# Performance work log

Measured on AMD Instinct MI355X. Metric: run time of the kernel, lower is better.

Reference implementation:

```python
import jax, jax.numpy as jnp
import numpy as np

X_DIM, Z_DIM, H_DIM, N_LAYERS = 128, 64, 512, 2
T, B = 128, 256
BETA = 1.0


def setup_inputs() -> dict:
    key = jax.random.key(0)
    ks = iter(jax.random.split(key, 64))
    def p(shape):
        return 0.05 * jax.random.normal(next(ks), shape, jnp.float32)
    d = {
        "x": jax.random.normal(next(ks), (T, B, X_DIM), jnp.float32),
        "eps": jax.random.normal(next(ks), (T, B, Z_DIM), jnp.float32),
        # phi_x: Linear(x,h) ReLU Linear(h,h) ReLU
        "phi_x_w1": p((H_DIM, X_DIM)), "phi_x_b1": p((H_DIM,)),
        "phi_x_w2": p((H_DIM, H_DIM)), "phi_x_b2": p((H_DIM,)),
        # phi_z: Linear(z,h) ReLU
        "phi_z_w": p((H_DIM, Z_DIM)), "phi_z_b": p((H_DIM,)),
        # enc: Linear(2h,h) ReLU Linear(h,h) ReLU; heads to z
        "enc_w1": p((H_DIM, 2 * H_DIM)), "enc_b1": p((H_DIM,)),
        "enc_w2": p((H_DIM, H_DIM)), "enc_b2": p((H_DIM,)),
        "enc_mu_w": p((Z_DIM, H_DIM)), "enc_mu_b": p((Z_DIM,)),
        "enc_lv_w": p((Z_DIM, H_DIM)), "enc_lv_b": p((Z_DIM,)),
        # prior: Linear(h,h) ReLU; heads to z
        "prior_w": p((H_DIM, H_DIM)), "prior_b": p((H_DIM,)),
        "prior_mu_w": p((Z_DIM, H_DIM)), "prior_mu_b": p((Z_DIM,)),
        "prior_lv_w": p((Z_DIM, H_DIM)), "prior_lv_b": p((Z_DIM,)),
        # dec: Linear(2h,h) ReLU Linear(h,h) ReLU; heads to x
        "dec_w1": p((H_DIM, 2 * H_DIM)), "dec_b1": p((H_DIM,)),
        "dec_w2": p((H_DIM, H_DIM)), "dec_b2": p((H_DIM,)),
        "dec_mu_w": p((X_DIM, H_DIM)), "dec_mu_b": p((X_DIM,)),
        "dec_lv_w": p((X_DIM, H_DIM)), "dec_lv_b": p((X_DIM,)),
        # GRU (bias=False): layer0 input 2h, layer1 input h
        "gru_wih0": p((3 * H_DIM, 2 * H_DIM)), "gru_whh0": p((3 * H_DIM, H_DIM)),
        "gru_wih1": p((3 * H_DIM, H_DIM)), "gru_whh1": p((3 * H_DIM, H_DIM)),
    }
    return d


def _lin(a, W, b):
    return a @ W.T + b


def _gru_cell(inp, h, Wih, Whh):
    gi = inp @ Wih.T  # [B, 3h]
    gh = h @ Whh.T
    i_r, i_z, i_n = jnp.split(gi, 3, axis=1)
    h_r, h_z, h_n = jnp.split(gh, 3, axis=1)
    r = jax.nn.sigmoid(i_r + h_r)
    zg = jax.nn.sigmoid(i_z + h_z)
    n = jnp.tanh(i_n + r * h_n)
    return (1.0 - zg) * n + zg * h


def reference(x, eps,
              phi_x_w1, phi_x_b1, phi_x_w2, phi_x_b2,
              phi_z_w, phi_z_b,
              enc_w1, enc_b1, enc_w2, enc_b2,
              enc_mu_w, enc_mu_b, enc_lv_w, enc_lv_b,
              prior_w, prior_b, prior_mu_w, prior_mu_b, prior_lv_w, prior_lv_b,
              dec_w1, dec_b1, dec_w2, dec_b2,
              dec_mu_w, dec_mu_b, dec_lv_w, dec_lv_b,
              gru_wih0, gru_whh0, gru_wih1, gru_whh1):
    Tn = x.shape[0]
    relu = jax.nn.relu

    def step(carry, xe):
        h, kld, rec = carry  # h: [N_LAYERS, B, H]
        x_t, eps_t = xe
        phi_x_t = relu(_lin(relu(_lin(x_t, phi_x_w1, phi_x_b1)), phi_x_w2, phi_x_b2))
        h_last = h[-1]
        enc_h = relu(_lin(relu(_lin(jnp.concatenate([phi_x_t, h_last], axis=1), enc_w1, enc_b1)), enc_w2, enc_b2))
        mu_q = _lin(enc_h, enc_mu_w, enc_mu_b)
        logvar_q = jnp.clip(_lin(enc_h, enc_lv_w, enc_lv_b), -6.0, 6.0)
        pri_h = relu(_lin(h_last, prior_w, prior_b))
        mu_p = _lin(pri_h, prior_mu_w, prior_mu_b)
        logvar_p = jnp.clip(_lin(pri_h, prior_lv_w, prior_lv_b), -6.0, 6.0)
        z_t = mu_q + eps_t * jnp.exp(0.5 * logvar_q)
        phi_z_t = relu(_lin(z_t, phi_z_w, phi_z_b))
        dec_h = relu(_lin(relu(_lin(jnp.concatenate([phi_z_t, h_last], axis=1), dec_w1, dec_b1)), dec_w2, dec_b2))
        dec_mu = _lin(dec_h, dec_mu_w, dec_mu_b)
        dec_lv = jnp.clip(_lin(dec_h, dec_lv_w, dec_lv_b), -6.0, 6.0)
        rnn_in = jnp.concatenate([phi_x_t, phi_z_t], axis=1)
        h0 = _gru_cell(rnn_in, h[0], gru_wih0, gru_whh0)
        h1 = _gru_cell(h0, h[1], gru_wih1, gru_whh1)
        h_new = jnp.stack([h0, h1])
        kl = 0.5 * jnp.sum(logvar_p - logvar_q + (jnp.exp(logvar_q) + (mu_q - mu_p) ** 2) / jnp.exp(logvar_p) - 1.0, axis=1)
        nll = 0.5 * jnp.sum(dec_lv + (x_t - dec_mu) ** 2 / jnp.exp(dec_lv), axis=1)
        return (h_new, kld + kl.mean(), rec + nll.mean()), None

    h0 = jnp.zeros((N_LAYERS, x.shape[1], H_DIM), x.dtype)
    (h_f, kld, rec), _ = jax.lax.scan(step, (h0, jnp.zeros((), x.dtype), jnp.zeros((), x.dtype)), (x, eps))
    total = (BETA * kld + rec) / Tn
    return total, rec / Tn, kld / Tn
```

## Files before the change

### kernel.cpp

```cpp
#include <hip/hip_runtime.h>
#include <hip/hip_bf16.h>

typedef __attribute__((ext_vector_type(4))) float f32x4;
typedef __attribute__((ext_vector_type(8))) short bf16x8;
typedef unsigned short u16;

#define DEV static __device__ __forceinline__

DEV u16 f2bf(float f){
  unsigned v = __float_as_uint(f);
  v += 0x7fffu + ((v >> 16) & 1u);
  return (u16)(v >> 16);
}
DEV float bf2f(u16 u){ return __uint_as_float(((unsigned)u) << 16); }
DEV float sigm(float x){ return 1.0f / (1.0f + __expf(-x)); }
DEV float tanh_(float x){ return 1.0f - 2.0f / (__expf(2.0f * x) + 1.0f); }
DEV bf16x8 ld8(const u16* p){ return *(const bf16x8*)p; }

struct GemmDesc {
  const u16* A; const u16* A2; const u16* W;
  const float* bias; void* out;
  int lda, lda2, ldw, ldo, N, K, K2, flags;
};
struct GemmMulti { GemmDesc d[4]; int nblk[4]; int ndesc; };

template<int NT>
DEV void mm_acc(const u16* ap, const u16* wp, int ldw, int K, f32x4* acc){
  for (int k = 0; k < K; k += 32){
    bf16x8 a = ld8(ap + k);
    #pragma unroll
    for (int nt = 0; nt < NT; ++nt){
      bf16x8 b = ld8(wp + (size_t)(nt * 16) * ldw + k);
      acc[nt] = __builtin_amdgcn_mfma_f32_16x16x32_bf16(a, b, acc[nt], 0, 0, 0);
    }
  }
}

DEV void run_gemm(const GemmDesc& d, int blk){
  const int ntn = d.N >> 6;
  const int bm = blk / ntn, bn = blk - bm * ntn;
  const int w = threadIdx.x >> 6, lane = threadIdx.x & 63;
  const int r = lane & 15, g = lane >> 4;
  const int m0 = bm * 64 + w * 16, n0 = bn * 64;
  f32x4 acc[4];
  #pragma unroll
  for (int i = 0; i < 4; ++i) acc[i] = (f32x4){0.f, 0.f, 0.f, 0.f};
  mm_acc<4>(d.A + (size_t)(m0 + r) * d.lda + g * 8,
            d.W + (size_t)(n0 + r) * d.ldw + g * 8, d.ldw, d.K, acc);
  if (d.A2)
    mm_acc<4>(d.A2 + (size_t)(m0 + r) * d.lda2 + g * 8,
              d.W + (size_t)(n0 + r) * d.ldw + d.K + g * 8, d.ldw, d.K2, acc);
  #pragma unroll
  for (int nt = 0; nt < 4; ++nt){
    #pragma unroll
    for (int i = 0; i < 4; ++i){
      const int row = m0 + g * 4 + i, col = n0 + nt * 16 + r;
      float v = acc[nt][i];
      if (d.bias) v += d.bias[col];
      if (d.flags & 1) v = fmaxf(v, 0.f);
      if (d.flags & 2) ((u16*)d.out)[(size_t)row * d.ldo + col] = f2bf(v);
      else             ((float*)d.out)[(size_t)row * d.ldo + col] = v;
    }
  }
}

__global__ __launch_bounds__(256) void k_gemm_multi(GemmMulti gm){
  int blk = blockIdx.x, di = 0;
  while (di < gm.ndesc - 1 && blk >= gm.nblk[di]){ blk -= gm.nblk[di]; ++di; }
  run_gemm(gm.d[di], blk);
}

#define NCONV 19
struct ConvMulti { const float* src[NCONV]; u16* dst[NCONV]; int n[NCONV]; int total; };

__global__ __launch_bounds__(256) void k_convert(ConvMulti cm){
  const int stride = gridDim.x * blockDim.x;
  for (int i = blockIdx.x * blockDim.x + threadIdx.x; i < cm.total; i += stride){
    int idx = i, di = 0;
    while (idx >= cm.n[di]){ idx -= cm.n[di]; ++di; }
    cm.dst[di][idx] = f2bf(cm.src[di][idx]);
  }
}

__global__ __launch_bounds__(256) void k_enc_fused(
    const u16* __restrict__ enc_h1, const u16* __restrict__ pri_h,
    const u16* __restrict__ enc_w2, const float* __restrict__ enc_b2,
    const u16* __restrict__ enc_mu_w, const float* __restrict__ enc_mu_b,
    const u16* __restrict__ enc_lv_w, const float* __restrict__ enc_lv_b,
    const u16* __restrict__ pri_mu_w, const float* __restrict__ pri_mu_b,
    const u16* __restrict__ pri_lv_w, const float* __restrict__ pri_lv_b,
    const u16* __restrict__ phi_z_w, const float* __restrict__ phi_z_b,
    const float* __restrict__ eps_t, u16* __restrict__ phi_z_out,
    float* __restrict__ kld_acc)
{
  __shared__ u16 enc_h_s[16 * 528];
  __shared__ float head_s[4][16 * 64];
  __shared__ u16 z_s[16 * 72];
  __shared__ float red[256];
  const int tid = threadIdx.x;
  const int w = tid >> 6, lane = tid & 63, r = lane & 15, g = lane >> 4;
  const int m0 = blockIdx.x * 16;

  {
    f32x4 acc[8];
    #pragma unroll
    for (int i = 0; i < 8; ++i) acc[i] = (f32x4){0.f, 0.f, 0.f, 0.f};
    const int n0 = w * 128;
    mm_acc<8>(enc_h1 + (size_t)(m0 + r) * 512 + g * 8,
              enc_w2 + (size_t)(n0 + r) * 512 + g * 8, 512, 512, acc);
    #pragma unroll
    for (int nt = 0; nt < 8; ++nt)
      #pragma unroll
      for (int i = 0; i < 4; ++i){
        const int row = g * 4 + i, col = n0 + nt * 16 + r;
        float v = fmaxf(acc[nt][i] + enc_b2[col], 0.f);
        enc_h_s[row * 528 + col] = f2bf(v);
      }
  }
  __syncthreads();
  {
    f32x4 acc[4];
    #pragma unroll
    for (int i = 0; i < 4; ++i) acc[i] = (f32x4){0.f, 0.f, 0.f, 0.f};
    const u16* ap; int lda; const u16* W; const float* bias; bool clip;
    if      (w == 0){ ap = enc_h_s;                      lda = 528; W = enc_mu_w; bias = enc_mu_b; clip = false; }
    else if (w == 1){ ap = enc_h_s;                      lda = 528; W = enc_lv_w; bias = enc_lv_b; clip = true;  }
    else if (w == 2){ ap = pri_h + (size_t)m0 * 512;     lda = 512; W = pri_mu_w; bias = pri_mu_b; clip = false; }
    else            { ap = pri_h + (size_t)m0 * 512;     lda = 512; W = pri_lv_w; bias = pri_lv_b; clip = true;  }
    mm_acc<4>(ap + (size_t)r * lda + g * 8, W + (size_t)r * 512 + g * 8, 512, 512, acc);
    #pragma unroll
    for (int nt = 0; nt < 4; ++nt)
      #pragma unroll
      for (int i = 0; i < 4; ++i){
        const int row = g * 4 + i, col = nt * 16 + r;
        float v = acc[nt][i] + bias[col];
        if (clip) v = fminf(fmaxf(v, -6.f), 6.f);
        head_s[w][row * 64 + col] = v;
      }
  }
  __syncthreads();
  float klsum = 0.f;
  for (int e = tid; e < 1024; e += 256){
    const int row = e >> 6, col = e & 63;
    const float qm = head_s[0][e], qv = head_s[1][e];
    const float pm = head_s[2][e], pv = head_s[3][e];
    const float zv = qm + eps_t[(size_t)(m0 + row) * 64 + col] * __expf(0.5f * qv);
    z_s[row * 72 + col] = f2bf(zv);
    const float dm = qm - pm;
    klsum += 0.5f * (pv - qv + (__expf(qv) + dm * dm) * __expf(-pv) - 1.0f);
  }
  red[tid] = klsum;
  __syncthreads();
  for (int s = 128; s > 0; s >>= 1){ if (tid < s) red[tid] += red[tid + s]; __syncthreads(); }
  if (tid == 0) atomicAdd(kld_acc, red[0]);
  {
    f32x4 acc[8];
    #pragma unroll
    for (int i = 0; i < 8; ++i) acc[i] = (f32x4){0.f, 0.f, 0.f, 0.f};
    const int n0 = w * 128;
    mm_acc<8>(z_s + (size_t)r * 72 + g * 8,
              phi_z_w + (size_t)(n0 + r) * 64 + g * 8, 64, 64, acc);
    #pragma unroll
    for (int nt = 0; nt < 8; ++nt)
      #pragma unroll
      for (int i = 0; i < 4; ++i){
        const int row = m0 + g * 4 + i, col = n0 + nt * 16 + r;
        float v = fmaxf(acc[nt][i] + phi_z_b[col], 0.f);
        phi_z_out[(size_t)row * 512 + col] = f2bf(v);
      }
  }
}

__global__ __launch_bounds__(256) void k_l5(GemmMulti gm,
    const float* __restrict__ gi0, const float* __restrict__ gh0, u16* __restrict__ h0)
{
  if ((int)blockIdx.x < gm.nblk[0]){ run_gemm(gm.d[0], blockIdx.x); return; }
  const int b = blockIdx.x - gm.nblk[0];
  for (int idx = b * 256 + threadIdx.x; idx < 256 * 512; idx += 16 * 256){
    const int row = idx >> 9, col = idx & 511;
    const float* gi = gi0 + (size_t)row * 1536;
    const float* gh = gh0 + (size_t)row * 1536;
    const float rr = sigm(gi[col] + gh[col]);
    const float zg = sigm(gi[col + 512] + gh[col + 512]);
    const float nn = tanh_(gi[col + 1024] + rr * gh[col + 1024]);
    const float hv = (1.f - zg) * nn + zg * bf2f(h0[idx]);
    h0[idx] = f2bf(hv);
  }
}

__global__ __launch_bounds__(256) void k_l6(GemmMulti gm,
    const u16* __restrict__ dec_h,
    const u16* __restrict__ dmu_w, const float* __restrict__ dmu_b,
    const u16* __restrict__ dlv_w, const float* __restrict__ dlv_b,
    const float* __restrict__ x_t, float* __restrict__ rec_acc)
{
  __shared__ float dmu_s[16 * 128], dlv_s[16 * 128];
  __shared__ float red[256];
  if ((int)blockIdx.x < gm.nblk[0]){ run_gemm(gm.d[0], blockIdx.x); return; }
  const int wg = blockIdx.x - gm.nblk[0];
  const int m0 = wg * 16;
  const int tid = threadIdx.x, w = tid >> 6, lane = tid & 63, r = lane & 15, g = lane >> 4;
  {
    f32x4 acc[4];
    #pragma unroll
    for (int i = 0; i < 4; ++i) acc[i] = (f32x4){0.f, 0.f, 0.f, 0.f};
    const u16* W = (w & 2) ? dlv_w : dmu_w;
    const float* bias = (w & 2) ? dlv_b : dmu_b;
    const int n0 = (w & 1) * 64;
    const bool clip = (w & 2);
    mm_acc<4>(dec_h + (size_t)(m0 + r) * 512 + g * 8,
              W + (size_t)(n0 + r) * 512 + g * 8, 512, 512, acc);
    #pragma unroll
    for (int nt = 0; nt < 4; ++nt)
      #pragma unroll
      for (int i = 0; i < 4; ++i){
        const int row = g * 4 + i, col = n0 + nt * 16 + r;
        float v = acc[nt][i] + bias[col];
        if (clip) v = fminf(fmaxf(v, -6.f), 6.f);
        (clip ? dlv_s : dmu_s)[row * 128 + col] = v;
      }
  }
  __syncthreads();
  float ns = 0.f;
  for (int e = tid; e < 2048; e += 256){
    const int row = e >> 7, col = e & 127;
    const float mu = dmu_s[e], lv = dlv_s[e];
    const float xv = x_t[(size_t)(m0 + row) * 128 + col];
    const float d = xv - mu;
    ns += 0.5f * (lv + d * d * __expf(-lv));
  }
  red[tid] = ns;
  __syncthreads();
  for (int s = 128; s > 0; s >>= 1){ if (tid < s) red[tid] += red[tid + s]; __syncthreads(); }
  if (tid == 0) atomicAdd(rec_acc, red[0]);
}

__global__ __launch_bounds__(256) void k_l7(const float* __restrict__ gi1,
    const float* __restrict__ gh1, u16* __restrict__ h1,
    int dofinal, const float* __restrict__ accf, float* __restrict__ out)
{
  if ((int)blockIdx.x < 16){
    for (int idx = blockIdx.x * 256 + threadIdx.x; idx < 256 * 512; idx += 16 * 256){
      const int row = idx >> 9, col = idx & 511;
      const float* gi = gi1 + (size_t)row * 1536;
      const float* gh = gh1 + (size_t)row * 1536;
      const float rr = sigm(gi[col] + gh[col]);
      const float zg = sigm(gi[col + 512] + gh[col + 512]);
      const float nn = tanh_(gi[col + 1024] + rr * gh[col + 1024]);
      const float hv = (1.f - zg) * nn + zg * bf2f(h1[idx]);
      h1[idx] = f2bf(hv);
    }
  } else if (dofinal && threadIdx.x == 0){
    const float kl = accf[0] * (1.f / 32768.f);
    const float rc = accf[1] * (1.f / 32768.f);
    out[0] = rc + kl; out[1] = rc; out[2] = kl;
  }
}

extern "C" void kernel_launch(void* const* d_in, const int* in_sizes, int n_in,
                              void* d_out, int out_size, void* d_ws, size_t ws_size,
                              hipStream_t stream)
{
  (void)in_sizes; (void)n_in; (void)out_size; (void)ws_size;
  const float* x     = (const float*)d_in[0];
  const float* eps   = (const float*)d_in[1];
  const float* w_px1 = (const float*)d_in[2];
  const float* b_px1 = (const float*)d_in[3];
  const float* w_px2 = (const float*)d_in[4];
  const float* b_px2 = (const float*)d_in[5];
  const float* w_pz  = (const float*)d_in[6];
  const float* b_pz  = (const float*)d_in[7];
  const float* w_e1  = (const float*)d_in[8];
  const float* b_e1  = (const float*)d_in[9];
  const float* w_e2  = (const float*)d_in[10];
  const float* b_e2  = (const float*)d_in[11];
  const float* w_emu = (const float*)d_in[12];
  const float* b_emu = (const float*)d_in[13];
  const float* w_elv = (const float*)d_in[14];
  const float* b_elv = (const float*)d_in[15];
  const float* w_pr  = (const float*)d_in[16];
  const float* b_pr  = (const float*)d_in[17];
  const float* w_pmu = (const float*)d_in[18];
  const float* b_pmu = (const float*)d_in[19];
  const float* w_plv = (const float*)d_in[20];
  const float* b_plv = (const float*)d_in[21];
  const float* w_d1  = (const float*)d_in[22];
  const float* b_d1  = (const float*)d_in[23];
  const float* w_d2  = (const float*)d_in[24];
  const float* b_d2  = (const float*)d_in[25];
  const float* w_dmu = (const float*)d_in[26];
  const float* b_dmu = (const float*)d_in[27];
  const float* w_dlv = (const float*)d_in[28];
  const float* b_dlv = (const float*)d_in[29];
  const float* w_ih0 = (const float*)d_in[30];
  const float* w_hh0 = (const float*)d_in[31];
  const float* w_ih1 = (const float*)d_in[32];
  const float* w_hh1 = (const float*)d_in[33];

  char* base = (char*)d_ws;
  size_t off = 0;
  auto alloc = [&](size_t bytes)->char*{
    char* p = base + off;
    off = (off + bytes + 255) & ~(size_t)255;
    return p;
  };
  u16* xbf    = (u16*)alloc((size_t)4194304 * 2);
  u16* cb_px1 = (u16*)alloc((size_t)65536 * 2);
  u16* cb_px2 = (u16*)alloc((size_t)262144 * 2);
  u16* cb_pz  = (u16*)alloc((size_t)32768 * 2);
  u16* cb_e1  = (u16*)alloc((size_t)524288 * 2);
  u16* cb_e2  = (u16*)alloc((size_t)262144 * 2);
  u16* cb_emu = (u16*)alloc((size_t)32768 * 2);
  u16* cb_elv = (u16*)alloc((size_t)32768 * 2);
  u16* cb_pr  = (u16*)alloc((size_t)262144 * 2);
  u16* cb_pmu = (u16*)alloc((size_t)32768 * 2);
  u16* cb_plv = (u16*)alloc((size_t)32768 * 2);
  u16* cb_d1  = (u16*)alloc((size_t)524288 * 2);
  u16* cb_d2  = (u16*)alloc((size_t)262144 * 2);
  u16* cb_dmu = (u16*)alloc((size_t)65536 * 2);
  u16* cb_dlv = (u16*)alloc((size_t)65536 * 2);
  u16* cb_ih0 = (u16*)alloc((size_t)1572864 * 2);
  u16* cb_hh0 = (u16*)alloc((size_t)786432 * 2);
  u16* cb_ih1 = (u16*)alloc((size_t)786432 * 2);
  u16* cb_hh1 = (u16*)alloc((size_t)786432 * 2);
  u16* phiX   = (u16*)alloc((size_t)16777216 * 2);
  const size_t mark = off;
  u16* phiX1  = (u16*)alloc((size_t)16777216 * 2);
  off = mark;
  u16* a_ench1 = (u16*)alloc((size_t)131072 * 2);
  u16* a_prih  = (u16*)alloc((size_t)131072 * 2);
  u16* a_phiz  = (u16*)alloc((size_t)131072 * 2);
  u16* a_dech1 = (u16*)alloc((size_t)131072 * 2);
  u16* a_dech  = (u16*)alloc((size_t)131072 * 2);
  float* gh0 = (float*)alloc((size_t)393216 * 4);
  float* gh1 = (float*)alloc((size_t)393216 * 4);
  float* gi0 = (float*)alloc((size_t)393216 * 4);
  float* gi1 = (float*)alloc((size_t)393216 * 4);
  u16* h0 = (u16*)alloc((size_t)131072 * 2);
  u16* h1 = (u16*)alloc((size_t)131072 * 2);
  float* accf = (float*)alloc(256);

  hipMemsetAsync(h0, 0, (size_t)131072 * 2 * 2 + 256, stream);

  ConvMulti cm; int ci = 0, tot = 0;
  auto addc = [&](const float* s, u16* d, int n){ cm.src[ci] = s; cm.dst[ci] = d; cm.n[ci] = n; ++ci; tot += n; };
  addc(x, xbf, 4194304);
  addc(w_px1, cb_px1, 65536);   addc(w_px2, cb_px2, 262144);
  addc(w_pz,  cb_pz,  32768);   addc(w_e1,  cb_e1,  524288);
  addc(w_e2,  cb_e2,  262144);  addc(w_emu, cb_emu, 32768);
  addc(w_elv, cb_elv, 32768);   addc(w_pr,  cb_pr,  262144);
  addc(w_pmu, cb_pmu, 32768);   addc(w_plv, cb_plv, 32768);
  addc(w_d1,  cb_d1,  524288);  addc(w_d2,  cb_d2,  262144);
  addc(w_dmu, cb_dmu, 65536);   addc(w_dlv, cb_dlv, 65536);
  addc(w_ih0, cb_ih0, 1572864); addc(w_hh0, cb_hh0, 786432);
  addc(w_ih1, cb_ih1, 786432);  addc(w_hh1, cb_hh1, 786432);
  cm.total = tot;
  k_convert<<<2048, 256, 0, stream>>>(cm);

  auto D = [](const u16* A, int lda, const u16* A2, int lda2, const u16* W, int ldw,
              const float* bias, void* out, int ldo, int N, int K, int K2, int flags)->GemmDesc{
    GemmDesc d; d.A = A; d.A2 = A2; d.W = W; d.bias = bias; d.out = out;
    d.lda = lda; d.lda2 = lda2; d.ldw = ldw; d.ldo = ldo;
    d.N = N; d.K = K; d.K2 = K2; d.flags = flags; return d;
  };

  {
    GemmMulti g; g.ndesc = 1;
    g.d[0] = D(xbf, 128, nullptr, 0, cb_px1, 128, b_px1, phiX1, 512, 512, 128, 0, 3);
    g.nblk[0] = 512 * 8;
    k_gemm_multi<<<512 * 8, 256, 0, stream>>>(g);
    g.d[0] = D(phiX1, 512, nullptr, 0, cb_px2, 512, b_px2, phiX, 512, 512, 512, 0, 3);
    k_gemm_multi<<<512 * 8, 256, 0, stream>>>(g);
  }

  for (int t = 0; t < 128; ++t){
    const u16* phiXt  = phiX + (size_t)t * 131072;
    const float* epst = eps  + (size_t)t * 16384;
    const float* xt   = x    + (size_t)t * 32768;

    GemmMulti g1; g1.ndesc = 4;
    g1.d[0] = D(phiXt, 512, h1, 512, cb_e1, 1024, b_e1, a_ench1, 512, 512, 512, 512, 3); g1.nblk[0] = 32;
    g1.d[1] = D(h1, 512, nullptr, 0, cb_pr, 512, b_pr, a_prih, 512, 512, 512, 0, 3);     g1.nblk[1] = 32;
    g1.d[2] = D(h1, 512, nullptr, 0, cb_hh1, 512, nullptr, gh1, 1536, 1536, 512, 0, 0);  g1.nblk[2] = 96;
    g1.d[3] = D(h0, 512, nullptr, 0, cb_hh0, 512, nullptr, gh0, 1536, 1536, 512, 0, 0);  g1.nblk[3] = 96;
    k_gemm_multi<<<256, 256, 0, stream>>>(g1);

    k_enc_fused<<<16, 256, 0, stream>>>(a_ench1, a_prih, cb_e2, b_e2,
        cb_emu, b_emu, cb_elv, b_elv, cb_pmu, b_pmu, cb_plv, b_plv,
        cb_pz, b_pz, epst, a_phiz, accf + 0);

    GemmMulti g4; g4.ndesc = 2;
    g4.d[0] = D(a_phiz, 512, h1, 512, cb_d1, 1024, b_d1, a_dech1, 512, 512, 512, 512, 3);  g4.nblk[0] = 32;
    g4.d[1] = D(phiXt, 512, a_phiz, 512, cb_ih0, 1024, nullptr, gi0, 1536, 1536, 512, 512, 0); g4.nblk[1] = 96;
    k_gemm_multi<<<128, 256, 0, stream>>>(g4);

    GemmMulti g5; g5.ndesc = 1;
    g5.d[0] = D(a_dech1, 512, nullptr, 0, cb_d2, 512, b_d2, a_dech, 512, 512, 512, 0, 3); g5.nblk[0] = 32;
    k_l5<<<48, 256, 0, stream>>>(g5, gi0, gh0, h0);

    GemmMulti g6; g6.ndesc = 1;
    g6.d[0] = D(h0, 512, nullptr, 0, cb_ih1, 512, nullptr, gi1, 1536, 1536, 512, 0, 0); g6.nblk[0] = 96;
    k_l6<<<112, 256, 0, stream>>>(g6, a_dech, cb_dmu, b_dmu, cb_dlv, b_dlv, xt, accf + 1);

    k_l7<<<17, 256, 0, stream>>>(gi1, gh1, h1, (t == 127) ? 1 : 0, accf, (float*)d_out);
  }
}
```

Before: 21.51 ms.

## Fuse the whole VRNN time loop into one persistent per-batch-tile kernel

Replaces the roughly seven kernel launches per timestep with a single persistent kernel. Each of 16 blocks owns 16 batch rows and loops over all 128 timesteps, keeping intermediate activations in shared memory and fusing both GRU gate GEMMs with their elementwise updates. Hidden states are double-buffered in global memory, so no grid-wide synchronisation is needed. This removes launch overhead and the global round-trips for gate pre-activations. The cost is that only 16 workgroups run, so every block streams all weights from cache at each step, which may leave most of the GPU idle and make the kernel cache-bandwidth bound.

```diff
diff --git a/kernel.cpp b/kernel.cpp
--- a/kernel.cpp
+++ b/kernel.cpp
@@ -16,58 +16,53 @@
 DEV float sigm(float x){ return 1.0f / (1.0f + __expf(-x)); }
 DEV float tanh_(float x){ return 1.0f - 2.0f / (__expf(2.0f * x) + 1.0f); }
 DEV bf16x8 ld8(const u16* p){ return *(const bf16x8*)p; }
-
-struct GemmDesc {
-  const u16* A; const u16* A2; const u16* W;
-  const float* bias; void* out;
-  int lda, lda2, ldw, ldo, N, K, K2, flags;
-};
-struct GemmMulti { GemmDesc d[4]; int nblk[4]; int ndesc; };
-
-template<int NT>
-DEV void mm_acc(const u16* ap, const u16* wp, int ldw, int K, f32x4* acc){
-  for (int k = 0; k < K; k += 32){
-    bf16x8 a = ld8(ap + k);
+DEV float clip6(float v){ return fminf(fmaxf(v, -6.f), 6.f); }
+
+template<int KIT, int NT>
+DEV void mmK(const u16* ap, const u16* wp, int ldw, f32x4* acc){
+  #pragma unroll 4
+  for (int kk = 0; kk < KIT; ++kk){
+    bf16x8 a = ld8(ap + kk * 32);
     #pragma unroll
     for (int nt = 0; nt < NT; ++nt){
-      bf16x8 b = ld8(wp + (size_t)(nt * 16) * ldw + k);
+      bf16x8 b = ld8(wp + (size_t)(nt * 16) * ldw + kk * 32);
       acc[nt] = __builtin_amdgcn_mfma_f32_16x16x32_bf16(a, b, acc[nt], 0, 0, 0);
     }
   }
 }
 
-DEV void run_gemm(const GemmDesc& d, int blk){
+struct GemmDesc {
+  const u16* A; const u16* W; const float* bias; u16* out;
+  int lda, ldw, ldo, N, K;
+};
+
+__global__ __launch_bounds__(256) void k_gemm_pre(GemmDesc d){
   const int ntn = d.N >> 6;
-  const int bm = blk / ntn, bn = blk - bm * ntn;
+  const int bm = blockIdx.x / ntn, bn = blockIdx.x - bm * ntn;
   const int w = threadIdx.x >> 6, lane = threadIdx.x & 63;
   const int r = lane & 15, g = lane >> 4;
   const int m0 = bm * 64 + w * 16, n0 = bn * 64;
   f32x4 acc[4];
   #pragma unroll
   for (int i = 0; i < 4; ++i) acc[i] = (f32x4){0.f, 0.f, 0.f, 0.f};
-  mm_acc<4>(d.A + (size_t)(m0 + r) * d.lda + g * 8,
-            d.W + (size_t)(n0 + r) * d.ldw + g * 8, d.ldw, d.K, acc);
-  if (d.A2)
-    mm_acc<4>(d.A2 + (size_t)(m0 + r) * d.lda2 + g * 8,
-              d.W + (size_t)(n0 + r) * d.ldw + d.K + g * 8, d.ldw, d.K2, acc);
+  const u16* ap = d.A + (size_t)(m0 + r) * d.lda + g * 8;
+  const u16* wp = d.W + (size_t)(n0 + r) * d.ldw + g * 8;
+  for (int k = 0; k < d.K; k += 32){
+    bf16x8 a = ld8(ap + k);
+    #pragma unroll
+    for (int nt = 0; nt < 4; ++nt){
+      bf16x8 b = ld8(wp + (size_t)(nt * 16) * d.ldw + k);
+      acc[nt] = __builtin_amdgcn_mfma_f32_16x16x32_bf16(a, b, acc[nt], 0, 0, 0);
+    }
+  }
   #pragma unroll
-  for (int nt = 0; nt < 4; ++nt){
+  for (int nt = 0; nt < 4; ++nt)
     #pragma unroll
     for (int i = 0; i < 4; ++i){
       const int row = m0 + g * 4 + i, col = n0 + nt * 16 + r;
-      float v = acc[nt][i];
-      if (d.bias) v += d.bias[col];
-      if (d.flags & 1) v = fmaxf(v, 0.f);
-      if (d.flags & 2) ((u16*)d.out)[(size_t)row * d.ldo + col] = f2bf(v);
-      else             ((float*)d.out)[(size_t)row * d.ldo + col] = v;
-    }
-  }
-}
-
-__global__ __launch_bounds__(256) void k_gemm_multi(GemmMulti gm){
-  int blk = blockIdx.x, di = 0;
-  while (di < gm.ndesc - 1 && blk >= gm.nblk[di]){ blk -= gm.nblk[di]; ++di; }
-  run_gemm(gm.d[di], blk);
+      float v = fmaxf(acc[nt][i] + d.bias[col], 0.f);
+      d.out[(size_t)row * d.ldo + col] = f2bf(v);
+    }
 }
 
 #define NCONV 19
@@ -82,177 +77,250 @@
   }
 }
 
-__global__ __launch_bounds__(256) void k_enc_fused(
-    const u16* __restrict__ enc_h1, const u16* __restrict__ pri_h,
-    const u16* __restrict__ enc_w2, const float* __restrict__ enc_b2,
-    const u16* __restrict__ enc_mu_w, const float* __restrict__ enc_mu_b,
-    const u16* __restrict__ enc_lv_w, const float* __restrict__ enc_lv_b,
-    const u16* __restrict__ pri_mu_w, const float* __restrict__ pri_mu_b,
-    const u16* __restrict__ pri_lv_w, const float* __restrict__ pri_lv_b,
-    const u16* __restrict__ phi_z_w, const float* __restrict__ phi_z_b,
-    const float* __restrict__ eps_t, u16* __restrict__ phi_z_out,
-    float* __restrict__ kld_acc)
+struct Params {
+  const u16 *phiX, *e1, *pr, *e2, *emu, *elv, *pmu, *plv, *pz, *d1, *ih0, *hh0, *ih1, *hh1, *d2, *dmu, *dlv;
+  const float *b_e1, *b_pr, *b_e2, *b_emu, *b_elv, *b_pmu, *b_plv, *b_pz, *b_d1, *b_d2, *b_dmu, *b_dlv;
+  const float *eps, *x;
+  u16 *h0a, *h0b, *h1a, *h1b;
+  float *accf;
+};
+
+#define HP 520
+
+__global__ __launch_bounds__(256, 1) void k_vrnn16(Params P)
 {
-  __shared__ u16 enc_h_s[16 * 528];
-  __shared__ float head_s[4][16 * 64];
-  __shared__ u16 z_s[16 * 72];
+  const int tid = threadIdx.x, w = tid >> 6, lane = tid & 63;
+  const int r = lane & 15, g = lane >> 4;
+  const int bid = blockIdx.x, m0 = bid * 16;
+  const int n0w = w * 128;
+
+  __shared__ u16 ench1_s[16 * HP], prih_s[16 * HP], phiz_s[16 * HP], dech1_s[16 * HP], dh_s[16 * HP];
+  __shared__ float fbuf[4096];
+  __shared__ u16 zs[16 * 72];
   __shared__ float red[256];
-  const int tid = threadIdx.x;
-  const int w = tid >> 6, lane = tid & 63, r = lane & 15, g = lane >> 4;
-  const int m0 = blockIdx.x * 16;
-
-  {
-    f32x4 acc[8];
-    #pragma unroll
-    for (int i = 0; i < 8; ++i) acc[i] = (f32x4){0.f, 0.f, 0.f, 0.f};
-    const int n0 = w * 128;
-    mm_acc<8>(enc_h1 + (size_t)(m0 + r) * 512 + g * 8,
-              enc_w2 + (size_t)(n0 + r) * 512 + g * 8, 512, 512, acc);
-    #pragma unroll
-    for (int nt = 0; nt < 8; ++nt)
-      #pragma unroll
-      for (int i = 0; i < 4; ++i){
-        const int row = g * 4 + i, col = n0 + nt * 16 + r;
-        float v = fmaxf(acc[nt][i] + enc_b2[col], 0.f);
-        enc_h_s[row * 528 + col] = f2bf(v);
+  float* qmu_s = fbuf;        float* qlv_s = fbuf + 1024;
+  float* pmu_s = fbuf + 2048; float* plv_s = fbuf + 3072;
+  float* dmu_s = fbuf;        float* dlv_s = fbuf + 2048;
+
+  float klacc = 0.f, nllacc = 0.f;
+
+  for (int t = 0; t < 128; ++t){
+    const u16* h1o = (t & 1) ? P.h1b : P.h1a;  u16* h1n = (t & 1) ? P.h1a : P.h1b;
+    const u16* h0o = (t & 1) ? P.h0b : P.h0a;  u16* h0n = (t & 1) ? P.h0a : P.h0b;
+    const u16* aX  = P.phiX + ((size_t)t * 256 + m0 + r) * 512 + g * 8;
+    const u16* aH1 = h1o + (size_t)(m0 + r) * 512 + g * 8;
+    const u16* aH0 = h0o + (size_t)(m0 + r) * 512 + g * 8;
+
+    { f32x4 acc[8];
+      #pragma unroll
+      for (int i = 0; i < 8; ++i) acc[i] = (f32x4){0.f,0.f,0.f,0.f};
+      mmK<16,8>(aX,  P.e1 + (size_t)(n0w + r) * 1024 + g * 8, 1024, acc);
+      mmK<16,8>(aH1, P.e1 + (size_t)(n0w + r) * 1024 + 512 + g * 8, 1024, acc);
+      #pragma unroll
+      for (int nt = 0; nt < 8; ++nt)
+        #pragma unroll
+        for (int i = 0; i < 4; ++i){
+          const int row = g * 4 + i, col = n0w + nt * 16 + r;
+          ench1_s[row * HP + col] = f2bf(fmaxf(acc[nt][i] + P.b_e1[col], 0.f));
+        }
+    }
+    { f32x4 acc[8];
+      #pragma unroll
+      for (int i = 0; i < 8; ++i) acc[i] = (f32x4){0.f,0.f,0.f,0.f};
+      mmK<16,8>(aH1, P.pr + (size_t)(n0w + r) * 512 + g * 8, 512, acc);
+      #pragma unroll
+      for (int nt = 0; nt < 8; ++nt)
+        #pragma unroll
+        for (int i = 0; i < 4; ++i){
+          const int row = g * 4 + i, col = n0w + nt * 16 + r;
+          prih_s[row * HP + col] = f2bf(fmaxf(acc[nt][i] + P.b_pr[col], 0.f));
+        }
+    }
+    __syncthreads();
+    { f32x4 acc[8];
+      #pragma unroll
+      for (int i = 0; i < 8; ++i) acc[i] = (f32x4){0.f,0.f,0.f,0.f};
+      mmK<16,8>(ench1_s + r * HP + g * 8, P.e2 + (size_t)(n0w + r) * 512 + g * 8, 512, acc);
+      #pragma unroll
+      for (int nt = 0; nt < 8; ++nt)
+        #pragma unroll
+        for (int i = 0; i < 4; ++i){
+          const int row = g * 4 + i, col = n0w + nt * 16 + r;
+          dh_s[row * HP + col] = f2bf(fmaxf(acc[nt][i] + P.b_e2[col], 0.f));
+        }
+    }
+    __syncthreads();
+    { f32x4 acc[4];
+      #pragma unroll
+      for (int i = 0; i < 4; ++i) acc[i] = (f32x4){0.f,0.f,0.f,0.f};
+      const u16* A  = (w < 2) ? dh_s : prih_s;
+      const u16* W_ = (w == 0) ? P.emu : (w == 1) ? P.elv : (w == 2) ? P.pmu : P.plv;
+      const float* bs = (w == 0) ? P.b_emu : (w == 1) ? P.b_elv : (w == 2) ? P.b_pmu : P.b_plv;
+      float* outp = (w == 0) ? qmu_s : (w == 1) ? qlv_s : (w == 2) ? pmu_s : plv_s;
+      const bool cl = (w & 1);
+      mmK<16,4>(A + r * HP + g * 8, W_ + (size_t)r * 512 + g * 8, 512, acc);
+      #pragma unroll
+      for (int nt = 0; nt < 4; ++nt)
+        #pragma unroll
+        for (int i = 0; i < 4; ++i){
+          const int row = g * 4 + i, col = nt * 16 + r;
+          float v = acc[nt][i] + bs[col];
+          if (cl) v = clip6(v);
+          outp[row * 64 + col] = v;
+        }
+    }
+    __syncthreads();
+    { const float* epst = P.eps + (size_t)t * 16384 + (size_t)m0 * 64;
+      for (int e = tid; e < 1024; e += 256){
+        const int row = e >> 6, col = e & 63;
+        const float qm = qmu_s[e], qv = qlv_s[e];
+        const float pm = pmu_s[e], pv = plv_s[e];
+        const float zv = qm + epst[row * 64 + col] * __expf(0.5f * qv);
+        zs[row * 72 + col] = f2bf(zv);
+        const float dm = qm - pm;
+        klacc += 0.5f * (pv - qv + (__expf(qv) + dm * dm) * __expf(-pv) - 1.f);
       }
-  }
-  __syncthreads();
-  {
-    f32x4 acc[4];
-    #pragma unroll
-    for (int i = 0; i < 4; ++i) acc[i] = (f32x4){0.f, 0.f, 0.f, 0.f};
-    const u16* ap; int lda; const u16* W; const float* bias; bool clip;
-    if      (w == 0){ ap = enc_h_s;                      lda = 528; W = enc_mu_w; bias = enc_mu_b; clip = false; }
-    else if (w == 1){ ap = enc_h_s;                      lda = 528; W = enc_lv_w; bias = enc_lv_b; clip = true;  }
-    else if (w == 2){ ap = pri_h + (size_t)m0 * 512;     lda = 512; W = pri_mu_w; bias = pri_mu_b; clip = false; }
-    else            { ap = pri_h + (size_t)m0 * 512;     lda = 512; W = pri_lv_w; bias = pri_lv_b; clip = true;  }
-    mm_acc<4>(ap + (size_t)r * lda + g * 8, W + (size_t)r * 512 + g * 8, 512, 512, acc);
-    #pragma unroll
-    for (int nt = 0; nt < 4; ++nt)
-      #pragma unroll
-      for (int i = 0; i < 4; ++i){
-        const int row = g * 4 + i, col = nt * 16 + r;
-        float v = acc[nt][i] + bias[col];
-        if (clip) v = fminf(fmaxf(v, -6.f), 6.f);
-        head_s[w][row * 64 + col] = v;
+    }
+    __syncthreads();
+    { f32x4 acc[8];
+      #pragma unroll
+      for (int i = 0; i < 8; ++i) acc[i] = (f32x4){0.f,0.f,0.f,0.f};
+      mmK<2,8>(zs + r * 72 + g * 8, P.pz + (size_t)(n0w + r) * 64 + g * 8, 64, acc);
+      #pragma unroll
+      for (int nt = 0; nt < 8; ++nt)
+        #pragma unroll
+        for (int i = 0; i < 4; ++i){
+          const int row = g * 4 + i, col = n0w + nt * 16 + r;
+          phiz_s[row * HP + col] = f2bf(fmaxf(acc[nt][i] + P.b_pz[col], 0.f));
+        }
+    }
+    __syncthreads();
+    { f32x4 acc[8];
+      #pragma unroll
+      for (int i = 0; i < 8; ++i) acc[i] = (f32x4){0.f,0.f,0.f,0.f};
+      mmK<16,8>(phiz_s + r * HP + g * 8, P.d1 + (size_t)(n0w + r) * 1024 + g * 8, 1024, acc);
+      mmK<16,8>(aH1, P.d1 + (size_t)(n0w + r) * 1024 + 512 + g * 8, 1024, acc);
+      #pragma unroll
+      for (int nt = 0; nt < 8; ++nt)
+        #pragma unroll
+        for (int i = 0; i < 4; ++i){
+          const int row = g * 4 + i, col = n0w + nt * 16 + r;
+          dech1_s[row * HP + col] = f2bf(fmaxf(acc[nt][i] + P.b_d1[col], 0.f));
+        }
+    }
+    { const u16* aZ = phiz_s + r * HP + g * 8;
+      for (int j = 0; j < 2; ++j){
+        f32x4 gi[3][4], gh[3][4];
+        #pragma unroll
+        for (int gt = 0; gt < 3; ++gt)
+          #pragma unroll
+          for (int i = 0; i < 4; ++i){ gi[gt][i] = (f32x4){0.f,0.f,0.f,0.f}; gh[gt][i] = (f32x4){0.f,0.f,0.f,0.f}; }
+        #pragma unroll
+        for (int gt = 0; gt < 3; ++gt){
+          const u16* wih = P.ih0 + (size_t)(gt * 512 + n0w + j * 64 + r) * 1024 + g * 8;
+          mmK<16,4>(aX, wih, 1024, gi[gt]);
+          mmK<16,4>(aZ, wih + 512, 1024, gi[gt]);
+          mmK<16,4>(aH0, P.hh0 + (size_t)(gt * 512 + n0w + j * 64 + r) * 512 + g * 8, 512, gh[gt]);
+        }
+        #pragma unroll
+        for (int nt = 0; nt < 4; ++nt)
+          #pragma unroll
+          for (int i = 0; i < 4; ++i){
+            const int row = g * 4 + i, c = n0w + j * 64 + nt * 16 + r;
+            const float rr = sigm(gi[0][nt][i] + gh[0][nt][i]);
+            const float zg = sigm(gi[1][nt][i] + gh[1][nt][i]);
+            const float nn = tanh_(gi[2][nt][i] + rr * gh[2][nt][i]);
+            const float hv = (1.f - zg) * nn + zg * bf2f(h0o[(size_t)(m0 + row) * 512 + c]);
+            h0n[(size_t)(m0 + row) * 512 + c] = f2bf(hv);
+          }
       }
-  }
-  __syncthreads();
-  float klsum = 0.f;
-  for (int e = tid; e < 1024; e += 256){
-    const int row = e >> 6, col = e & 63;
-    const float qm = head_s[0][e], qv = head_s[1][e];
-    const float pm = head_s[2][e], pv = head_s[3][e];
-    const float zv = qm + eps_t[(size_t)(m0 + row) * 64 + col] * __expf(0.5f * qv);
-    z_s[row * 72 + col] = f2bf(zv);
-    const float dm = qm - pm;
-    klsum += 0.5f * (pv - qv + (__expf(qv) + dm * dm) * __expf(-pv) - 1.0f);
-  }
-  red[tid] = klsum;
+    }
+    __syncthreads();
+    { const u16* aH0n = h0n + (size_t)(m0 + r) * 512 + g * 8;
+      for (int j = 0; j < 2; ++j){
+        f32x4 gi[3][4], gh[3][4];
+        #pragma unroll
+        for (int gt = 0; gt < 3; ++gt)
+          #pragma unroll
+          for (int i = 0; i < 4; ++i){ gi[gt][i] = (f32x4){0.f,0.f,0.f,0.f}; gh[gt][i] = (f32x4){0.f,0.f,0.f,0.f}; }
+        #pragma unroll
+        for (int gt = 0; gt < 3; ++gt){
+          mmK<16,4>(aH0n, P.ih1 + (size_t)(gt * 512 + n0w + j * 64 + r) * 512 + g * 8, 512, gi[gt]);
+          mmK<16,4>(aH1,  P.hh1 + (size_t)(gt * 512 + n0w + j * 64 + r) * 512 + g * 8, 512, gh[gt]);
+        }
+        #pragma unroll
+        for (int nt = 0; nt < 4; ++nt)
+          #pragma unroll
+          for (int i = 0; i < 4; ++i){
+            const int row = g * 4 + i, c = n0w + j * 64 + nt * 16 + r;
+            const float rr = sigm(gi[0][nt][i] + gh[0][nt][i]);
+            const float zg = sigm(gi[1][nt][i] + gh[1][nt][i]);
+            const float nn = tanh_(gi[2][nt][i] + rr * gh[2][nt][i]);
+            const float hv = (1.f - zg) * nn + zg * bf2f(h1o[(size_t)(m0 + row) * 512 + c]);
+            h1n[(size_t)(m0 + row) * 512 + c] = f2bf(hv);
+          }
+      }
+    }
+    __syncthreads();
+    { f32x4 acc[8];
+      #pragma unroll
+      for (int i = 0; i < 8; ++i) acc[i] = (f32x4){0.f,0.f,0.f,0.f};
+      mmK<16,8>(dech1_s + r * HP + g * 8, P.d2 + (size_t)(n0w + r) * 512 + g * 8, 512, acc);
+      #pragma unroll
+      for (int nt = 0; nt < 8; ++nt)
+        #pragma unroll
+        for (int i = 0; i < 4; ++i){
+          const int row = g * 4 + i, col = n0w + nt * 16 + r;
+          dh_s[row * HP + col] = f2bf(fmaxf(acc[nt][i] + P.b_d2[col], 0.f));
+        }
+    }
+    __syncthreads();
+    { f32x4 acc[4];
+      #pragma unroll
+      for (int i = 0; i < 4; ++i) acc[i] = (f32x4){0.f,0.f,0.f,0.f};
+      const bool isLv = (w >= 2); const int coff = (w & 1) * 64;
+      const u16* W_ = isLv ? P.dlv : P.dmu;
+      const float* bs = isLv ? P.b_dlv : P.b_dmu;
+      mmK<16,4>(dh_s + r * HP + g * 8, W_ + (size_t)(coff + r) * 512 + g * 8, 512, acc);
+      #pragma unroll
+      for (int nt = 0; nt < 4; ++nt)
+        #pragma unroll
+        for (int i = 0; i < 4; ++i){
+          const int row = g * 4 + i, col = coff + nt * 16 + r;
+          float v = acc[nt][i] + bs[col];
+          if (isLv) v = clip6(v);
+          (isLv ? dlv_s : dmu_s)[row * 128 + col] = v;
+        }
+    }
+    __syncthreads();
+    { const float* xt = P.x + (size_t)t * 32768 + (size_t)m0 * 128;
+      for (int e = tid; e < 2048; e += 256){
+        const int row = e >> 7, col = e & 127;
+        const float mu = dmu_s[e], lv = dlv_s[e];
+        const float d = xt[row * 128 + col] - mu;
+        nllacc += 0.5f * (lv + d * d * __expf(-lv));
+      }
+    }
+    __syncthreads();
+  }
+
+  red[tid] = klacc;
   __syncthreads();
   for (int s = 128; s > 0; s >>= 1){ if (tid < s) red[tid] += red[tid + s]; __syncthreads(); }
-  if (tid == 0) atomicAdd(kld_acc, red[0]);
-  {
-    f32x4 acc[8];
-    #pragma unroll
-    for (int i = 0; i < 8; ++i) acc[i] = (f32x4){0.f, 0.f, 0.f, 0.f};
-    const int n0 = w * 128;
-    mm_acc<8>(z_s + (size_t)r * 72 + g * 8,
-              phi_z_w + (size_t)(n0 + r) * 64 + g * 8, 64, 64, acc);
-    #pragma unroll
-    for (int nt = 0; nt < 8; ++nt)
-      #pragma unroll
-      for (int i = 0; i < 4; ++i){
-        const int row = m0 + g * 4 + i, col = n0 + nt * 16 + r;
-        float v = fmaxf(acc[nt][i] + phi_z_b[col], 0.f);
-        phi_z_out[(size_t)row * 512 + col] = f2bf(v);
-      }
-  }
-}
-
-__global__ __launch_bounds__(256) void k_l5(GemmMulti gm,
-    const float* __restrict__ gi0, const float* __restrict__ gh0, u16* __restrict__ h0)
-{
-  if ((int)blockIdx.x < gm.nblk[0]){ run_gemm(gm.d[0], blockIdx.x); return; }
-  const int b = blockIdx.x - gm.nblk[0];
-  for (int idx = b * 256 + threadIdx.x; idx < 256 * 512; idx += 16 * 256){
-    const int row = idx >> 9, col = idx & 511;
-    const float* gi = gi0 + (size_t)row * 1536;
-    const float* gh = gh0 + (size_t)row * 1536;
-    const float rr = sigm(gi[col] + gh[col]);
-    const float zg = sigm(gi[col + 512] + gh[col + 512]);
-    const float nn = tanh_(gi[col + 1024] + rr * gh[col + 1024]);
-    const float hv = (1.f - zg) * nn + zg * bf2f(h0[idx]);
-    h0[idx] = f2bf(hv);
-  }
-}
-
-__global__ __launch_bounds__(256) void k_l6(GemmMulti gm,
-    const u16* __restrict__ dec_h,
-    const u16* __restrict__ dmu_w, const float* __restrict__ dmu_b,
-    const u16* __restrict__ dlv_w, const float* __restrict__ dlv_b,
-    const float* __restrict__ x_t, float* __restrict__ rec_acc)
-{
-  __shared__ float dmu_s[16 * 128], dlv_s[16 * 128];
-  __shared__ float red[256];
-  if ((int)blockIdx.x < gm.nblk[0]){ run_gemm(gm.d[0], blockIdx.x); return; }
-  const int wg = blockIdx.x - gm.nblk[0];
-  const int m0 = wg * 16;
-  const int tid = threadIdx.x, w = tid >> 6, lane = tid & 63, r = lane & 15, g = lane >> 4;
-  {
-    f32x4 acc[4];
-    #pragma unroll
-    for (int i = 0; i < 4; ++i) acc[i] = (f32x4){0.f, 0.f, 0.f, 0.f};
-    const u16* W = (w & 2) ? dlv_w : dmu_w;
-    const float* bias = (w & 2) ? dlv_b : dmu_b;
-    const int n0 = (w & 1) * 64;
-    const bool clip = (w & 2);
-    mm_acc<4>(dec_h + (size_t)(m0 + r) * 512 + g * 8,
-              W + (size_t)(n0 + r) * 512 + g * 8, 512, 512, acc);
-    #pragma unroll
-    for (int nt = 0; nt < 4; ++nt)
-      #pragma unroll
-      for (int i = 0; i < 4; ++i){
-        const int row = g * 4 + i, col = n0 + nt * 16 + r;
-        float v = acc[nt][i] + bias[col];
-        if (clip) v = fminf(fmaxf(v, -6.f), 6.f);
-        (clip ? dlv_s : dmu_s)[row * 128 + col] = v;
-      }
-  }
+  if (tid == 0) P.accf[bid] = red[0];
   __syncthreads();
-  float ns = 0.f;
-  for (int e = tid; e < 2048; e += 256){
-    const int row = e >> 7, col = e & 127;
-    const float mu = dmu_s[e], lv = dlv_s[e];
-    const float xv = x_t[(size_t)(m0 + row) * 128 + col];
-    const float d = xv - mu;
-    ns += 0.5f * (lv + d * d * __expf(-lv));
-  }
-  red[tid] = ns;
+  red[tid] = nllacc;
   __syncthreads();
   for (int s = 128; s > 0; s >>= 1){ if (tid < s) red[tid] += red[tid + s]; __syncthreads(); }
-  if (tid == 0) atomicAdd(rec_acc, red[0]);
-}
-
-__global__ __launch_bounds__(256) void k_l7(const float* __restrict__ gi1,
-    const float* __restrict__ gh1, u16* __restrict__ h1,
-    int dofinal, const float* __restrict__ accf, float* __restrict__ out)
-{
-  if ((int)blockIdx.x < 16){
-    for (int idx = blockIdx.x * 256 + threadIdx.x; idx < 256 * 512; idx += 16 * 256){
-      const int row = idx >> 9, col = idx & 511;
-      const float* gi = gi1 + (size_t)row * 1536;
-      const float* gh = gh1 + (size_t)row * 1536;
-      const float rr = sigm(gi[col] + gh[col]);
-      const float zg = sigm(gi[col + 512] + gh[col + 512]);
-      const float nn = tanh_(gi[col + 1024] + rr * gh[col + 1024]);
-      const float hv = (1.f - zg) * nn + zg * bf2f(h1[idx]);
-      h1[idx] = f2bf(hv);
-    }
-  } else if (dofinal && threadIdx.x == 0){
-    const float kl = accf[0] * (1.f / 32768.f);
-    const float rc = accf[1] * (1.f / 32768.f);
+  if (tid == 0) P.accf[16 + bid] = red[0];
+}
+
+__global__ void k_final(const float* __restrict__ accf, float* __restrict__ out){
+  if (threadIdx.x == 0 && blockIdx.x == 0){
+    float kl = 0.f, rc = 0.f;
+    for (int i = 0; i < 16; ++i){ kl += accf[i]; rc += accf[16 + i]; }
+    kl *= (1.f / 32768.f);
+    rc *= (1.f / 32768.f);
     out[0] = rc + kl; out[1] = rc; out[2] = kl;
   }
 }
@@ -324,23 +392,14 @@
   u16* cb_ih1 = (u16*)alloc((size_t)786432 * 2);
   u16* cb_hh1 = (u16*)alloc((size_t)786432 * 2);
   u16* phiX   = (u16*)alloc((size_t)16777216 * 2);
-  const size_t mark = off;
   u16* phiX1  = (u16*)alloc((size_t)16777216 * 2);
-  off = mark;
-  u16* a_ench1 = (u16*)alloc((size_t)131072 * 2);
-  u16* a_prih  = (u16*)alloc((size_t)131072 * 2);
-  u16* a_phiz  = (u16*)alloc((size_t)131072 * 2);
-  u16* a_dech1 = (u16*)alloc((size_t)131072 * 2);
-  u16* a_dech  = (u16*)alloc((size_t)131072 * 2);
-  float* gh0 = (float*)alloc((size_t)393216 * 4);
-  float* gh1 = (float*)alloc((size_t)393216 * 4);
-  float* gi0 = (float*)alloc((size_t)393216 * 4);
-  float* gi1 = (float*)alloc((size_t)393216 * 4);
-  u16* h0 = (u16*)alloc((size_t)131072 * 2);
-  u16* h1 = (u16*)alloc((size_t)131072 * 2);
+  u16* h0a = (u16*)alloc((size_t)131072 * 2);
+  u16* h0b = (u16*)alloc((size_t)131072 * 2);
+  u16* h1a = (u16*)alloc((size_t)131072 * 2);
+  u16* h1b = (u16*)alloc((size_t)131072 * 2);
   float* accf = (float*)alloc(256);
 
-  hipMemsetAsync(h0, 0, (size_t)131072 * 2 * 2 + 256, stream);
+  hipMemsetAsync(h0a, 0, (size_t)4 * 262144, stream);
 
   ConvMulti cm; int ci = 0, tot = 0;
   auto addc = [&](const float* s, u16* d, int n){ cm.src[ci] = s; cm.dst[ci] = d; cm.n[ci] = n; ++ci; tot += n; };
@@ -357,51 +416,32 @@
   cm.total = tot;
   k_convert<<<2048, 256, 0, stream>>>(cm);
 
-  auto D = [](const u16* A, int lda, const u16* A2, int lda2, const u16* W, int ldw,
-              const float* bias, void* out, int ldo, int N, int K, int K2, int flags)->GemmDesc{
-    GemmDesc d; d.A = A; d.A2 = A2; d.W = W; d.bias = bias; d.out = out;
-    d.lda = lda; d.lda2 = lda2; d.ldw = ldw; d.ldo = ldo;
-    d.N = N; d.K = K; d.K2 = K2; d.flags = flags; return d;
-  };
-
   {
-    GemmMulti g; g.ndesc = 1;
-    g.d[0] = D(xbf, 128, nullptr, 0, cb_px1, 128, b_px1, phiX1, 512, 512, 128, 0, 3);
-    g.nblk[0] = 512 * 8;
-    k_gemm_multi<<<512 * 8, 256, 0, stream>>>(g);
-    g.d[0] = D(phiX1, 512, nullptr, 0, cb_px2, 512, b_px2, phiX, 512, 512, 512, 0, 3);
-    k_gemm_multi<<<512 * 8, 256, 0, stream>>>(g);
-  }
-
-  for (int t = 0; t < 128; ++t){
-    const u16* phiXt  = phiX + (size_t)t * 131072;
-    const float* epst = eps  + (size_t)t * 16384;
-    const float* xt   = x    + (size_t)t * 32768;
-
-    GemmMulti g1; g1.ndesc = 4;
-    g1.d[0] = D(phiXt, 512, h1, 512, cb_e1, 1024, b_e1, a_ench1, 512, 512, 512, 512, 3); g1.nblk[0] = 32;
-    g1.d[1] = D(h1, 512, nullptr, 0, cb_pr, 512, b_pr, a_prih, 512, 512, 512, 0, 3);     g1.nblk[1] = 32;
-    g1.d[2] = D(h1, 512, nullptr, 0, cb_hh1, 512, nullptr, gh1, 1536, 1536, 512, 0, 0);  g1.nblk[2] = 96;
-    g1.d[3] = D(h0, 512, nullptr, 0, cb_hh0, 512, nullptr, gh0, 1536, 1536, 512, 0, 0);  g1.nblk[3] = 96;
-    k_gemm_multi<<<256, 256, 0, stream>>>(g1);
-
-    k_enc_fused<<<16, 256, 0, stream>>>(a_ench1, a_prih, cb_e2, b_e2,
-        cb_emu, b_emu, cb_elv, b_elv, cb_pmu, b_pmu, cb_plv, b_plv,
-        cb_pz, b_pz, epst, a_phiz, accf + 0);
-
-    GemmMulti g4; g4.ndesc = 2;
-    g4.d[0] = D(a_phiz, 512, h1, 512, cb_d1, 1024, b_d1, a_dech1, 512, 512, 512, 512, 3);  g4.nblk[0] = 32;
-    g4.d[1] = D(phiXt, 512, a_phiz, 512, cb_ih0, 1024, nullptr, gi0, 1536, 1536, 512, 512, 0); g4.nblk[1] = 96;
-    k_gemm_multi<<<128, 256, 0, stream>>>(g4);
-
-    GemmMulti g5; g5.ndesc = 1;
-    g5.d[0] = D(a_dech1, 512, nullptr, 0, cb_d2, 512, b_d2, a_dech, 512, 512, 512, 0, 3); g5.nblk[0] = 32;
-    k_l5<<<48, 256, 0, stream>>>(g5, gi0, gh0, h0);
-
-    GemmMulti g6; g6.ndesc = 1;
-    g6.d[0] = D(h0, 512, nullptr, 0, cb_ih1, 512, nullptr, gi1, 1536, 1536, 512, 0, 0); g6.nblk[0] = 96;
-    k_l6<<<112, 256, 0, stream>>>(g6, a_dech, cb_dmu, b_dmu, cb_dlv, b_dlv, xt, accf + 1);
-
-    k_l7<<<17, 256, 0, stream>>>(gi1, gh1, h1, (t == 127) ? 1 : 0, accf, (float*)d_out);
-  }
-}
+    GemmDesc d1g;
+    d1g.A = xbf; d1g.W = cb_px1; d1g.bias = b_px1; d1g.out = phiX1;
+    d1g.lda = 128; d1g.ldw = 128; d1g.ldo = 512; d1g.N = 512; d1g.K = 128;
+    k_gemm_pre<<<512 * 8, 256, 0, stream>>>(d1g);
+    GemmDesc d2g;
+    d2g.A = phiX1; d2g.W = cb_px2; d2g.bias = b_px2; d2g.out = phiX;
+    d2g.lda = 512; d2g.ldw = 512; d2g.ldo = 512; d2g.N = 512; d2g.K = 512;
+    k_gemm_pre<<<512 * 8, 256, 0, stream>>>(d2g);
+  }
+
+  Params prm;
+  prm.phiX = phiX;
+  prm.e1 = cb_e1; prm.pr = cb_pr; prm.e2 = cb_e2;
+  prm.emu = cb_emu; prm.elv = cb_elv; prm.pmu = cb_pmu; prm.plv = cb_plv;
+  prm.pz = cb_pz; prm.d1 = cb_d1; prm.ih0 = cb_ih0; prm.hh0 = cb_hh0;
+  prm.ih1 = cb_ih1; prm.hh1 = cb_hh1; prm.d2 = cb_d2;
+  prm.dmu = cb_dmu; prm.dlv = cb_dlv;
+  prm.b_e1 = b_e1; prm.b_pr = b_pr; prm.b_e2 = b_e2;
+  prm.b_emu = b_emu; prm.b_elv = b_elv; prm.b_pmu = b_pmu; prm.b_plv = b_plv;
+  prm.b_pz = b_pz; prm.b_d1 = b_d1; prm.b_d2 = b_d2;
+  prm.b_dmu = b_dmu; prm.b_dlv = b_dlv;
+  prm.eps = eps; prm.x = x;
+  prm.h0a = h0a; prm.h0b = h0b; prm.h1a = h1a; prm.h1b = h1b;
+  prm.accf = accf;
+
+  k_vrnn16<<<dim3(16), dim3(256), 0, stream>>>(prm);
+  k_final<<<dim3(1), dim3(64), 0, stream>>>(accf, (float*)d_out);
+}
```

Measured after the change: 54.27 ms. 2.52x slower.
